# Optimization experiments

Measured on AMD Instinct MI355X. Metric: run time of the kernel, lower is better.

Reference implementation:

```python
import math
import jax, jax.numpy as jnp
import numpy as np

N, S, E, H = 8, 1024, 768, 12  # batch, seq_len, n_embed, n_head


def setup_inputs() -> dict:
    key = jax.random.key(0)
    ks = jax.random.split(key, 10)
    s = 1.0 / math.sqrt(E)
    x = jax.random.normal(ks[0], (N, S, E), dtype=jnp.float32)
    # per-head full-width projections, stacked over heads: [H, E, E] (Linear weight layout [out, in])
    Wq = jax.random.normal(ks[1], (H, E, E), dtype=jnp.float32) * s
    Wk = jax.random.normal(ks[2], (H, E, E), dtype=jnp.float32) * s
    Wv = jax.random.normal(ks[3], (H, E, E), dtype=jnp.float32) * s
    bq = jax.random.normal(ks[4], (H, E), dtype=jnp.float32) * s
    bk = jax.random.normal(ks[5], (H, E), dtype=jnp.float32) * s
    bv = jax.random.normal(ks[6], (H, E), dtype=jnp.float32) * s
    Wc = jax.random.normal(ks[7], (E, H * E), dtype=jnp.float32) * (1.0 / math.sqrt(H * E))
    bc = jax.random.normal(ks[8], (E,), dtype=jnp.float32) * s
    return {"x": x, "Wq": Wq, "bq": bq, "Wk": Wk, "bk": bk, "Wv": Wv, "bv": bv, "Wc": Wc, "bc": bc}


def reference(x, Wq, bq, Wk, bk, Wv, bv, Wc, bc):
    # Full-width QKV per head: [H, N, S, E]
    q = jnp.einsum('nse,hde->hnsd', x, Wq) + bq[:, None, None, :]
    k = jnp.einsum('nse,hde->hnsd', x, Wk) + bk[:, None, None, :]
    v = jnp.einsum('nse,hde->hnsd', x, Wv) + bv[:, None, None, :]
    # scores scaled by sqrt(n_embed) (source quirk: full n_embed, not head_dim)
    scores = jnp.einsum('hnsd,hntd->hnst', q, k) / math.sqrt(E)
    causal = jnp.tril(jnp.ones((S, S), dtype=bool))
    scores = jnp.where(causal[None, None, :, :], scores, -jnp.inf)
    # dropout applied before softmax in source; p=0 (eval) -> identity
    attn = jax.nn.softmax(scores, axis=-1)
    heads = jnp.einsum('hnst,hntd->hnsd', attn, v)  # [H, N, S, E]
    concat = jnp.transpose(heads, (1, 2, 0, 3)).reshape(N, S, H * E)
    return concat @ Wc.T + bc
```

## Files before the change

### kernel.cpp

```cpp
#include <hip/hip_runtime.h>
#include <hip/hip_bf16.h>
#include <stdint.h>

#define SEQ    1024
#define NBAT   8
#define EMB    768
#define NHEAD  12
#define MROWS  (NBAT*SEQ)
#define SCALE_S 0.03608439182435161f

typedef unsigned short u16;
typedef __attribute__((ext_vector_type(8))) short bf16x8;
typedef __attribute__((ext_vector_type(4))) float f32x4;

typedef void __attribute__((address_space(1)))* gas_ptr;
typedef void __attribute__((address_space(3)))* las_ptr;

__device__ __forceinline__ void gload16(const void* g, void* l) {
  __builtin_amdgcn_global_load_lds((gas_ptr)(void*)g, (las_ptr)l, 16, 0, 0);
}

#define VMCNT0 asm volatile("s_waitcnt vmcnt(0)" ::: "memory")
#define VMCNT2 asm volatile("s_waitcnt vmcnt(2)" ::: "memory")
#define VMCNT4 asm volatile("s_waitcnt vmcnt(4)" ::: "memory")
#define LGKM0  asm volatile("s_waitcnt lgkmcnt(0)" ::: "memory")
#define BARRIER asm volatile("s_barrier" ::: "memory")

__device__ __forceinline__ u16 f2bf(float f) {
  union { float f; uint32_t u; } a; a.f = f;
  uint32_t r = a.u + 0x7fffu + ((a.u >> 16) & 1u);
  return (u16)(r >> 16);
}
__device__ __forceinline__ uint32_t pack2(float a, float b) {
  return (uint32_t)f2bf(a) | ((uint32_t)f2bf(b) << 16);
}

__global__ void k_cvt(const float* __restrict__ s, u16* __restrict__ d, long n) {
  long i = ((long)blockIdx.x*blockDim.x + threadIdx.x)*8;
  if (i >= n) return;
  float4 a = *(const float4*)(s+i);
  float4 b = *(const float4*)(s+i+4);
  uint4 o; o.x = pack2(a.x,a.y); o.y = pack2(a.z,a.w);
  o.z = pack2(b.x,b.y); o.w = pack2(b.z,b.w);
  *(uint4*)(d+i) = o;
}

__global__ void k_cvt3(const float* __restrict__ s0, const float* __restrict__ s1,
                       const float* __restrict__ s2, u16* __restrict__ d0,
                       u16* __restrict__ d1, u16* __restrict__ d2, long n) {
  const float* s = blockIdx.z == 0 ? s0 : (blockIdx.z == 1 ? s1 : s2);
  u16* d = blockIdx.z == 0 ? d0 : (blockIdx.z == 1 ? d1 : d2);
  long i = ((long)blockIdx.x*blockDim.x + threadIdx.x)*8;
  if (i >= n) return;
  float4 a = *(const float4*)(s+i);
  float4 b = *(const float4*)(s+i+4);
  uint4 o; o.x = pack2(a.x,a.y); o.y = pack2(a.z,a.w);
  o.z = pack2(b.x,b.y); o.w = pack2(b.z,b.w);
  *(uint4*)(d+i) = o;
}

__global__ void k_cvtwc(const float* __restrict__ wc, u16* __restrict__ d, int Gi, int h0) {
  long ncol = (long)Gi*EMB;
  long i = ((long)blockIdx.x*blockDim.x + threadIdx.x)*4;
  if (i >= 768*ncol) return;
  long eo = i / ncol, c = i - eo*ncol;
  long g = c / EMB, dd = c - g*EMB;
  const float* s = wc + eo*(long)(NHEAD*EMB) + (h0+g)*EMB + dd;
  float4 a = *(const float4*)s;
  uint2 o; o.x = pack2(a.x,a.y); o.y = pack2(a.z,a.w);
  *(uint2*)(d+i) = o;
}

__global__ __launch_bounds__(512, 2) void k_gemm256(
    const u16* __restrict__ A, int lda,
    const u16* __restrict__ B, int ldb, int K,
    u16* __restrict__ Cb, long c_hs, int ldc,
    const float* __restrict__ bias, const float* __restrict__ bias2,
    int gsplit, int mode)
{
  __shared__ u16 lsA[2*16384];
  __shared__ u16 lsB[2*16384];

  int m0 = blockIdx.x * 256;
  int n0 = blockIdx.y * 256;
  int tid = threadIdx.x;
  int w = tid >> 6, l = tid & 63;
  int wr = w >> 2, wc = w & 3;

  const u16* gA = A + (size_t)(m0 + 32*w + (l>>3))*lda + (((l&7) ^ (l>>3)) << 3);
  const u16* gB = B + (size_t)(n0 + 32*w + (l>>3))*ldb + (((l&7) ^ (l>>3)) << 3);

#define STAGE256(t, buf) do { \
    int k0_ = (t)*64; \
    _Pragma("unroll") \
    for (int c_ = 0; c_ < 4; ++c_) \
      gload16(gA + (size_t)(c_*8)*lda + k0_, lsA + (buf)*16384 + (32*w + 8*c_)*64); \
    _Pragma("unroll") \
    for (int c_ = 0; c_ < 4; ++c_) \
      gload16(gB + (size_t)(c_*8)*ldb + k0_, lsB + (buf)*16384 + (32*w + 8*c_)*64); \
  } while(0)

  f32x4 acc[8][4];
  #pragma unroll
  for (int i = 0; i < 8; ++i)
    #pragma unroll
    for (int j = 0; j < 4; ++j) acc[i][j] = (f32x4)0.0f;

  int nt = K >> 6;
  STAGE256(0, 0);
  for (int t = 0; t < nt; ++t) {
    VMCNT0; BARRIER;
    if (t + 1 < nt) STAGE256(t+1, (t+1)&1);
    const u16* la = lsA + (t&1)*16384;
    const u16* lb = lsB + (t&1)*16384;
    #pragma unroll
    for (int ks = 0; ks < 2; ++ks) {
      int off = (((4*ks + (l>>4)) ^ (l&7)) << 3);
      bf16x8 af[8], bf_[4];
      #pragma unroll
      for (int fi = 0; fi < 8; ++fi)
        af[fi] = *(const bf16x8*)(la + (wr*128 + fi*16 + (l&15))*64 + off);
      #pragma unroll
      for (int fj = 0; fj < 4; ++fj)
        bf_[fj] = *(const bf16x8*)(lb + (wc*64 + fj*16 + (l&15))*64 + off);
      __builtin_amdgcn_s_setprio(1);
      #pragma unroll
      for (int fi = 0; fi < 8; ++fi)
        #pragma unroll
        for (int fj = 0; fj < 4; ++fj)
          acc[fi][fj] = __builtin_amdgcn_mfma_f32_16x16x32_bf16(af[fi], bf_[fj], acc[fi][fj], 0, 0, 0);
      __builtin_amdgcn_s_setprio(0);
    }
  }
#undef STAGE256

  if (mode == 0) {
    int s = n0 / 768;
    int dbase = n0 - s*768 + wc*64;
    const float* bsl = (s < gsplit) ? bias + (size_t)s*768 : bias2 + (size_t)(s - gsplit)*768;
    u16* Cs = Cb + (size_t)s*c_hs;
    #pragma unroll
    for (int fj = 0; fj < 4; ++fj) {
      int dcol = dbase + fj*16 + (l&15);
      float bb = bsl[dcol];
      #pragma unroll
      for (int fi = 0; fi < 8; ++fi) {
        #pragma unroll
        for (int r = 0; r < 4; ++r) {
          int row = m0 + wr*128 + fi*16 + (l>>4)*4 + r;
          Cs[(size_t)row*768 + dcol] = f2bf(acc[fi][fj][r] + bb);
        }
      }
    }
  } else {
    #pragma unroll
    for (int fi = 0; fi < 8; ++fi) {
      #pragma unroll
      for (int r = 0; r < 4; ++r) {
        int row = m0 + wr*128 + fi*16 + (l>>4)*4 + r;
        float bb = bias[row];
        #pragma unroll
        for (int fj = 0; fj < 4; ++fj) {
          int cbn = n0 + wc*64 + fj*16 + (l&15);
          Cb[(size_t)row*ldc + cbn] = f2bf(acc[fi][fj][r] + bb);
        }
      }
    }
  }
}

__global__ __launch_bounds__(256) void k_gemm(
    const u16* __restrict__ A, long a_hs, int lda,
    const u16* __restrict__ B, long b_hs, int ldb, int K,
    u16* Cb, float* Cf, long c_hs, int ldc,
    const float* __restrict__ bias, const float* __restrict__ bias2,
    long bias_hs, int gsplit, int mode, int swapxy)
{
  __shared__ u16 lsA[3*4096];
  __shared__ u16 lsB[3*4096];
  int g = blockIdx.z;
  const u16* Ag = A + (long)g*a_hs;
  const u16* Bg = B + (long)g*b_hs;
  int tm = swapxy ? blockIdx.y : blockIdx.x;
  int tn = swapxy ? blockIdx.x : blockIdx.y;
  int m0 = tm*128, n0 = tn*128;
  int tid = threadIdx.x;
  int w = tid >> 6, l = tid & 63;

  int srow = l >> 2;
  int scol = ((l & 3) ^ ((l >> 3) & 3)) * 8;
  const u16* ga0 = Ag + (long)(m0 + (2*w)*16   + srow)*lda + scol;
  const u16* ga1 = Ag + (long)(m0 + (2*w+1)*16 + srow)*lda + scol;
  const u16* gb0 = Bg + (long)(n0 + (2*w)*16   + srow)*ldb + scol;
  const u16* gb1 = Bg + (long)(n0 + (2*w+1)*16 + srow)*ldb + scol;

#define GSTAGE(k0, buf) do { \
    gload16(ga0 + (k0), lsA + (buf)*4096 + (2*w)*512); \
    gload16(ga1 + (k0), lsA + (buf)*4096 + (2*w+1)*512); \
    gload16(gb0 + (k0), lsB + (buf)*4096 + (2*w)*512); \
    gload16(gb1 + (k0), lsB + (buf)*4096 + (2*w+1)*512); \
  } while(0)

  f32x4 acc[4][4];
  #pragma unroll
  for (int i = 0; i < 4; ++i)
    #pragma unroll
    for (int j = 0; j < 4; ++j) acc[i][j] = (f32x4)0.0f;

  int wr = w >> 1, wc_ = w & 1;
  int frow = l & 15;
  int sp = (l >> 4) ^ ((frow >> 1) & 3);
  int aoff[4], boff[4];
  #pragma unroll
  for (int i = 0; i < 4; ++i) {
    aoff[i] = (wr*64 + i*16 + frow)*32 + sp*8;
    boff[i] = (wc_*64 + i*16 + frow)*32 + sp*8;
  }

  int nt = K >> 5;
  GSTAGE(0, 0);
  GSTAGE(32, 1);
  VMCNT4; BARRIER;
  int cur = 0;
  for (int t = 0; t < nt; ++t) {
    if (t + 2 < nt) {
      int nb = cur + 2; if (nb >= 3) nb -= 3;
      GSTAGE((t+2) << 5, nb);
    }
    const u16* la = lsA + cur*4096;
    const u16* lb = lsB + cur*4096;
    bf16x8 af[4], bfr[4];
    #pragma unroll
    for (int i = 0; i < 4; ++i) af[i] = *(const bf16x8*)(la + aoff[i]);
    #pragma unroll
    for (int j = 0; j < 4; ++j) bfr[j] = *(const bf16x8*)(lb + boff[j]);
    #pragma unroll
    for (int i = 0; i < 4; ++i)
      #pragma unroll
      for (int j = 0; j < 4; ++j)
        acc[i][j] = __builtin_amdgcn_mfma_f32_16x16x32_bf16(af[i], bfr[j], acc[i][j], 0, 0, 0);
    if (t + 2 < nt) { VMCNT4; } else { VMCNT0; }
    LGKM0; BARRIER;
    cur = (cur == 2) ? 0 : cur + 1;
  }
#undef GSTAGE

  u16* Cbg = Cb ? Cb + (long)g*c_hs : (u16*)0;
  const float* bsel = (g < gsplit) ? bias : bias2;
  long gi = (g < gsplit) ? g : g - gsplit;
  const float* bs = bsel ? bsel + gi*bias_hs : (const float*)0;
  int rl = (l >> 4)*4, cl = l & 15;
  #pragma unroll
  for (int i = 0; i < 4; ++i) {
    #pragma unroll
    for (int j = 0; j < 4; ++j) {
      int rb = m0 + wr*64 + i*16 + rl;
      int cb = n0 + wc_*64 + j*16 + cl;
      float cbv = 0.f;
      if ((mode == 0 || mode == 2) && bs) cbv = bs[cb];
      #pragma unroll
      for (int r = 0; r < 4; ++r) {
        int rr = rb + r;
        float v = acc[i][j][r];
        v += (mode == 1) ? bs[rr] : cbv;
        size_t idx = (size_t)rr*(size_t)ldc + cb;
        if (mode <= 1) Cbg[idx] = f2bf(v);
        else if (mode == 2) Cf[idx] = v;
        else Cf[idx] += v;
      }
    }
  }
}

__global__ __launch_bounds__(512, 2) void k_attn(
    const u16* __restrict__ qb, const u16* __restrict__ kb,
    const u16* __restrict__ vtb, u16* __restrict__ hb, int ldh)
{
  __shared__ u16 kls[3*8192];
  __shared__ u16 vls[3*8192];
  __shared__ float s_t[64*68];
  __shared__ u16 p_t[64*64];
  __shared__ float e_s[64];

  int b = blockIdx.x;
  int xcd = b & 7, kk_ = b >> 3;
  int gn = xcd + 8*(kk_ >> 3), pair = kk_ & 7;
  int g = gn >> 3, n = gn & 7;

  const u16* Q  = qb  + (size_t)g*MROWS*EMB + (size_t)n*SEQ*EMB;
  const u16* Kp = kb  + (size_t)g*MROWS*EMB + (size_t)n*SEQ*EMB;
  const u16* Vt = vtb + (size_t)g*EMB*MROWS + (size_t)n*SEQ;
  u16* H = hb + (size_t)(n*SEQ)*ldh + (size_t)g*EMB;

  int tid = threadIdx.x;
  int w = tid >> 6, l = tid & 63;
  int qg = w >> 1;
  int cg = w & 1;
  int frow = l & 15;
  int fsw = frow & 7;
  int srow = tid >> 3;
  int sphys = tid & 7;
  int scol = ((sphys ^ (srow & 7)) << 3);

#define KSTAGE(base, pc, buf) do { \
    gload16((base) + (pc)*128,      kls + (buf)*8192 + w*512); \
    gload16((base) + (pc)*128 + 64, kls + (buf)*8192 + 4096 + w*512); \
  } while(0)
#define VSTAGE(vc, buf) do { \
    gload16(Vs + (size_t)((vc)*128)*MROWS,      vls + (buf)*8192 + w*512); \
    gload16(Vs + (size_t)((vc)*128 + 64)*MROWS, vls + (buf)*8192 + 4096 + w*512); \
  } while(0)

  for (int half = 0; half < 2; ++half) {
    int qt = half ? 15 - pair : pair;
    int q0 = qt * 64;
    int nt = qt + 1;

    f32x4 acc[6][4];
    #pragma unroll
    for (int i = 0; i < 6; ++i)
      #pragma unroll
      for (int j = 0; j < 4; ++j) acc[i][j] = (f32x4)0.0f;
    float m_reg = -1e30f, l_reg = 0.f;

    const u16* Qs = Q + (size_t)(q0 + srow)*EMB + scol;
    bf16x8 qreg[12][2];
    KSTAGE(Qs, 0, 0);
    KSTAGE(Qs, 1, 1);
    VMCNT2; BARRIER;
    #pragma unroll
    for (int pc = 0; pc < 6; ++pc) {
      if (pc < 4) KSTAGE(Qs, pc+2, (pc+2)%3);
      const u16* qb_ = kls + (pc%3)*8192;
      #pragma unroll
      for (int kk2 = 0; kk2 < 2; ++kk2)
        #pragma unroll
        for (int kkl = 0; kkl < 2; ++kkl)
          qreg[2*pc + kk2][kkl] = *(const bf16x8*)(qb_ + kk2*4096 + (qg*16 + frow)*64
                                                   + (((kkl*4 + (l>>4)) ^ fsw) << 3));
      if (pc < 4) { VMCNT2; } else if (pc == 4) { VMCNT0; }
      LGKM0; BARRIER;
    }

    for (int tt = 0; tt < nt; ++tt) {
      int t0 = tt*64;
      const u16* Ks = Kp + (size_t)(t0 + srow)*EMB + scol;
      const u16* Vs = Vt + (size_t)srow*MROWS + t0 + scol;
      if (tt == 0) { KSTAGE(Ks, 0, 0); KSTAGE(Ks, 1, 1); }
      VMCNT2; BARRIER;

      f32x4 sacc[2]; sacc[0] = (f32x4)0.0f; sacc[1] = (f32x4)0.0f;
      #pragma unroll
      for (int c = 0; c < 6; ++c) {
        if (c < 4)       KSTAGE(Ks, c+2, (c+2)%3);
        else if (c == 4) VSTAGE(0, 0);
        else             VSTAGE(1, 1);
        const u16* kb_ = kls + (c%3)*8192;
        __builtin_amdgcn_s_setprio(1);
        #pragma unroll
        for (int kk2 = 0; kk2 < 2; ++kk2) {
          #pragma unroll
          for (int kkl = 0; kkl < 2; ++kkl) {
            int so = ((kkl*4 + (l>>4)) ^ fsw) << 3;
            bf16x8 aq = qreg[2*c + kk2][kkl];
            #pragma unroll
            for (int cc = 0; cc < 2; ++cc) {
              bf16x8 bk_ = *(const bf16x8*)(kb_ + kk2*4096 + ((cg*2 + cc)*16 + frow)*64 + so);
              sacc[cc] = __builtin_amdgcn_mfma_f32_16x16x32_bf16(aq, bk_, sacc[cc], 0, 0, 0);
            }
          }
        }
        __builtin_amdgcn_s_setprio(0);
        if (c < 5) { VMCNT2; LGKM0; BARRIER; }
      }

      #pragma unroll
      for (int cc = 0; cc < 2; ++cc)
        #pragma unroll
        for (int r = 0; r < 4; ++r)
          s_t[(qg*16 + (l>>4)*4 + r)*68 + cg*32 + cc*16 + (l&15)] = sacc[cc][r]*SCALE_S;
      LGKM0; BARRIER;
      {
        int qglob = q0 + srow;
        int cbase = t0 + sphys*8;
        float v[8]; float mx = -1e30f;
        #pragma unroll
        for (int j = 0; j < 8; ++j) {
          float s = s_t[srow*68 + sphys*8 + j];
          if (cbase + j > qglob) s = -1e30f;
          v[j] = s; mx = fmaxf(mx, s);
        }
        mx = fmaxf(mx, __shfl_xor(mx, 1));
        mx = fmaxf(mx, __shfl_xor(mx, 2));
        mx = fmaxf(mx, __shfl_xor(mx, 4));
        float mn = fmaxf(m_reg, mx);
        float esc = __expf(m_reg - mn);
        float ps = 0.f; u16 pk[8];
        #pragma unroll
        for (int j = 0; j < 8; ++j) { float p = __expf(v[j] - mn); ps += p; pk[j] = f2bf(p); }
        ps += __shfl_xor(ps, 1); ps += __shfl_xor(ps, 2); ps += __shfl_xor(ps, 4);
        l_reg = l_reg*esc + ps; m_reg = mn;
        if (sphys == 0) e_s[srow] = esc;
        uint4 pv;
        pv.x = (uint32_t)pk[0] | ((uint32_t)pk[1] << 16);
        pv.y = (uint32_t)pk[2] | ((uint32_t)pk[3] << 16);
        pv.z = (uint32_t)pk[4] | ((uint32_t)pk[5] << 16);
        pv.w = (uint32_t)pk[6] | ((uint32_t)pk[7] << 16);
        *(uint4*)(p_t + srow*64 + ((sphys ^ (srow & 7)) << 3)) = pv;
      }
      VMCNT2; LGKM0; BARRIER;
      float er[4];
      #pragma unroll
      for (int r = 0; r < 4; ++r) er[r] = e_s[qg*16 + (l>>4)*4 + r];
      #pragma unroll
      for (int i = 0; i < 6; ++i)
        #pragma unroll
        for (int j = 0; j < 4; ++j)
          #pragma unroll
          for (int r = 0; r < 4; ++r) acc[i][j][r] *= er[r];
      bf16x8 pa[2];
      #pragma unroll
      for (int kk = 0; kk < 2; ++kk)
        pa[kk] = *(const bf16x8*)(p_t + (qg*16 + frow)*64 + (((kk*4 + (l>>4)) ^ fsw) << 3));
      bool stage_next = (tt + 1 < nt);
      const u16* Ks2 = Kp + (size_t)(t0 + 64 + srow)*EMB + scol;
      #pragma unroll
      for (int c = 0; c < 6; ++c) {
        if (c < 4)            VSTAGE(c+2, (c+2)%3);
        else if (stage_next)  { if (c == 4) KSTAGE(Ks2, 0, 0); else KSTAGE(Ks2, 1, 1); }
        const u16* vb_ = vls + (c%3)*8192;
        __builtin_amdgcn_s_setprio(1);
        #pragma unroll
        for (int cf = 0; cf < 4; ++cf) {
          #pragma unroll
          for (int kk = 0; kk < 2; ++kk) {
            bf16x8 vbf = *(const bf16x8*)(vb_ + (cg*64 + cf*16 + frow)*64 + (((kk*4 + (l>>4)) ^ fsw) << 3));
            acc[c][cf] = __builtin_amdgcn_mfma_f32_16x16x32_bf16(pa[kk], vbf, acc[c][cf], 0, 0, 0);
          }
        }
        __builtin_amdgcn_s_setprio(0);
        if (c < 4)      { VMCNT2; LGKM0; BARRIER; }
        else if (c == 4){ if (stage_next) { VMCNT2; } else { VMCNT0; } LGKM0; BARRIER; }
      }
    }
    if (sphys == 0) e_s[srow] = l_reg;
    LGKM0; BARRIER;
    float linv[4];
    #pragma unroll
    for (int r = 0; r < 4; ++r) linv[r] = 1.0f / e_s[qg*16 + (l>>4)*4 + r];
    #pragma unroll
    for (int i = 0; i < 6; ++i)
      #pragma unroll
      for (int j = 0; j < 4; ++j) {
        int col = i*128 + cg*64 + j*16 + (l & 15);
        #pragma unroll
        for (int r = 0; r < 4; ++r) {
          int row = q0 + qg*16 + (l>>4)*4 + r;
          H[(size_t)row*ldh + col] = f2bf(acc[i][j][r]*linv[r]);
        }
      }
    BARRIER;
  }
#undef KSTAGE
#undef VSTAGE
}

extern "C" void kernel_launch(void* const* d_in, const int* in_sizes, int n_in,
                              void* d_out, int out_size, void* d_ws, size_t ws_size,
                              hipStream_t stream) {
  const float* x  = (const float*)d_in[0];
  const float* Wq = (const float*)d_in[1];
  const float* bq = (const float*)d_in[2];
  const float* Wk = (const float*)d_in[3];
  const float* bk = (const float*)d_in[4];
  const float* Wv = (const float*)d_in[5];
  const float* bv = (const float*)d_in[6];
  const float* Wc = (const float*)d_in[7];
  const float* bc = (const float*)d_in[8];
  float* out = (float*)d_out;

  const size_t XB  = (size_t)MROWS*EMB*sizeof(u16);
  const size_t WHB = (size_t)EMB*EMB*sizeof(u16);
  const size_t per_g = 4*WHB + 4*XB;
  long long avail = (long long)ws_size - (long long)XB - 4096;
  int G = (int)(avail / (long long)per_g);
  if (G < 1) G = 1;
  if (G > NHEAD) G = NHEAD;

  char* ws = (char*)d_ws;
  u16* xb  = (u16*)ws;  ws += XB;
  u16* wqb = (u16*)ws;  ws += (size_t)(2*G)*WHB;
  u16* wvb = (u16*)ws;  ws += (size_t)G*WHB;
  u16* wcb = (u16*)ws;  ws += (size_t)G*WHB;
  u16* qb  = (u16*)ws;  ws += (size_t)(2*G)*XB;
  u16* vtb = (u16*)ws;  ws += (size_t)G*XB;
  u16* hbf = (u16*)ws;  ws += (size_t)G*XB;

  k_cvt<<<dim3(3072), dim3(256), 0, stream>>>(x, xb, (long)MROWS*EMB);

  for (int h0 = 0; h0 < NHEAD; h0 += G) {
    int Gi = (G < NHEAD - h0) ? G : (NHEAD - h0);
    long nw = (long)Gi*EMB*EMB;
    k_cvt3<<<dim3((unsigned)(nw/8/256), 1, 3), dim3(256), 0, stream>>>(
        Wq + (size_t)h0*EMB*EMB, Wk + (size_t)h0*EMB*EMB, Wv + (size_t)h0*EMB*EMB,
        wqb, wqb + (size_t)Gi*EMB*EMB, wvb, nw);
    k_cvtwc<<<dim3((unsigned)((768L*Gi*EMB/4)/256)), dim3(256), 0, stream>>>(Wc, wcb, Gi, h0);
    k_gemm256<<<dim3(32, 6*Gi), dim3(512), 0, stream>>>(
        xb, EMB, wqb, EMB, EMB,
        qb, (long)MROWS*EMB, 768,
        bq + (size_t)h0*EMB, bk + (size_t)h0*EMB, Gi, 0);
    k_gemm256<<<dim3(3*Gi, 32), dim3(512), 0, stream>>>(
        wvb, EMB, xb, EMB, EMB,
        vtb, 0L, MROWS,
        bv + (size_t)h0*EMB, (const float*)0, 9999, 1);
    k_attn<<<dim3(8*NBAT*Gi), dim3(512), 0, stream>>>(
        qb, qb + (size_t)Gi*MROWS*EMB, vtb, hbf, Gi*EMB);
    k_gemm<<<dim3(64, 6, 1), dim3(256), 0, stream>>>(
        hbf, 0L, Gi*EMB, wcb, 0L, Gi*EMB, Gi*EMB,
        (u16*)0, out, 0L, EMB,
        (h0 == 0 ? bc : (const float*)0), (const float*)0, 0L, 9999,
        (h0 == 0 ? 2 : 3), 0);
  }
}
```

Measured before the change: 1.144 ms.

## Fold Wq^T·Wk into per-head matrix, skip K projection, drop key bias

Rewrites the scores algebraically as (x M + bq Wk) x^T with M = Wq^T Wk computed per head. The separate K projection GEMM goes away, keys come straight from the bf16 x, and the bq-dependent term becomes a per-key scalar added to the scores. Terms constant along each softmax row (bk and its cross terms) are dropped because softmax cancels them. This costs extra small kernels: a transposing weight conversion, a 768x768 M GEMM per head, and two GEMV kernels. Rounding M to bf16 may also change numerics.

```diff
diff --git a/kernel.cpp b/kernel.cpp
--- a/kernel.cpp
+++ b/kernel.cpp
@@ -30,6 +30,9 @@
   union { float f; uint32_t u; } a; a.f = f;
   uint32_t r = a.u + 0x7fffu + ((a.u >> 16) & 1u);
   return (u16)(r >> 16);
+}
+__device__ __forceinline__ float bf2f(u16 b) {
+  union { uint32_t u; float f; } c; c.u = (uint32_t)b << 16; return c.f;
 }
 __device__ __forceinline__ uint32_t pack2(float a, float b) {
   return (uint32_t)f2bf(a) | ((uint32_t)f2bf(b) << 16);
@@ -45,18 +48,27 @@
   *(uint4*)(d+i) = o;
 }
 
-__global__ void k_cvt3(const float* __restrict__ s0, const float* __restrict__ s1,
-                       const float* __restrict__ s2, u16* __restrict__ d0,
-                       u16* __restrict__ d1, u16* __restrict__ d2, long n) {
-  const float* s = blockIdx.z == 0 ? s0 : (blockIdx.z == 1 ? s1 : s2);
-  u16* d = blockIdx.z == 0 ? d0 : (blockIdx.z == 1 ? d1 : d2);
-  long i = ((long)blockIdx.x*blockDim.x + threadIdx.x)*8;
-  if (i >= n) return;
-  float4 a = *(const float4*)(s+i);
-  float4 b = *(const float4*)(s+i+4);
-  uint4 o; o.x = pack2(a.x,a.y); o.y = pack2(a.z,a.w);
-  o.z = pack2(b.x,b.y); o.w = pack2(b.z,b.w);
-  *(uint4*)(d+i) = o;
+__global__ void k_cvtT(const float* __restrict__ wq, const float* __restrict__ wk,
+                       u16* __restrict__ dq, u16* __restrict__ dk, int Gi) {
+  __shared__ float t[64][65];
+  int z = blockIdx.z;
+  const float* src = (z < Gi) ? wq + (size_t)z*EMB*EMB : wk + (size_t)(z-Gi)*EMB*EMB;
+  u16* dst = (z < Gi) ? dq + (size_t)z*EMB*EMB : dk + (size_t)(z-Gi)*EMB*EMB;
+  int d0 = blockIdx.x*64, e0 = blockIdx.y*64;
+  int tt = threadIdx.x;
+  int el = tt & 63, db = tt >> 6;
+  #pragma unroll
+  for (int p = 0; p < 16; ++p) {
+    int dl = p*4 + db;
+    t[dl][el] = src[(size_t)(d0+dl)*EMB + e0 + el];
+  }
+  __syncthreads();
+  int dl2 = tt & 63, eb = tt >> 6;
+  #pragma unroll
+  for (int p = 0; p < 16; ++p) {
+    int e2 = p*4 + eb;
+    dst[(size_t)(e0+e2)*EMB + d0 + dl2] = f2bf(t[dl2][e2]);
+  }
 }
 
 __global__ void k_cvtwc(const float* __restrict__ wc, u16* __restrict__ d, int Gi, int h0) {
@@ -71,6 +83,35 @@
   *(uint2*)(d+i) = o;
 }
 
+__global__ void k_mka(const u16* __restrict__ wkT, const float* __restrict__ bq,
+                      float* __restrict__ a) {
+  int g = blockIdx.y;
+  int e = blockIdx.x*256 + threadIdx.x;
+  const u16* row = wkT + (size_t)g*EMB*EMB + (size_t)e*EMB;
+  const float* b = bq + (size_t)g*EMB;
+  float s = 0.f;
+  for (int d = 0; d < EMB; ++d) s += bf2f(row[d]) * b[d];
+  a[(size_t)g*EMB + e] = s;
+}
+
+__global__ void k_mkv(const u16* __restrict__ xb, const float* __restrict__ a,
+                      float* __restrict__ v) {
+  int g = blockIdx.y;
+  int w = threadIdx.x >> 6, l = threadIdx.x & 63;
+  int i = blockIdx.x*8 + w;
+  const u16* xr = xb + (size_t)i*EMB;
+  const float* ag = a + (size_t)g*EMB;
+  float s = 0.f;
+  #pragma unroll
+  for (int c = 0; c < 12; ++c) {
+    int e = c*64 + l;
+    s += bf2f(xr[e]) * ag[e];
+  }
+  s += __shfl_xor(s, 1); s += __shfl_xor(s, 2); s += __shfl_xor(s, 4);
+  s += __shfl_xor(s, 8); s += __shfl_xor(s, 16); s += __shfl_xor(s, 32);
+  if (l == 0) v[(size_t)g*MROWS + i] = s;
+}
+
 __global__ __launch_bounds__(512, 2) void k_gemm256(
     const u16* __restrict__ A, int lda,
     const u16* __restrict__ B, int ldb, int K,
@@ -137,12 +178,14 @@
   if (mode == 0) {
     int s = n0 / 768;
     int dbase = n0 - s*768 + wc*64;
-    const float* bsl = (s < gsplit) ? bias + (size_t)s*768 : bias2 + (size_t)(s - gsplit)*768;
+    const float* bsl = bias ? ((s < gsplit) ? bias + (size_t)s*768
+                                            : bias2 + (size_t)(s - gsplit)*768)
+                            : (const float*)0;
     u16* Cs = Cb + (size_t)s*c_hs;
     #pragma unroll
     for (int fj = 0; fj < 4; ++fj) {
       int dcol = dbase + fj*16 + (l&15);
-      float bb = bsl[dcol];
+      float bb = bsl ? bsl[dcol] : 0.f;
       #pragma unroll
       for (int fi = 0; fi < 8; ++fi) {
         #pragma unroll
@@ -273,8 +316,9 @@
 }
 
 __global__ __launch_bounds__(512, 2) void k_attn(
-    const u16* __restrict__ qb, const u16* __restrict__ kb,
-    const u16* __restrict__ vtb, u16* __restrict__ hb, int ldh)
+    const u16* __restrict__ qb, const u16* __restrict__ xkb,
+    const u16* __restrict__ vtb, const float* __restrict__ vh,
+    u16* __restrict__ hb, int ldh)
 {
   __shared__ u16 kls[3*8192];
   __shared__ u16 vls[3*8192];
@@ -288,8 +332,9 @@
   int g = gn >> 3, n = gn & 7;
 
   const u16* Q  = qb  + (size_t)g*MROWS*EMB + (size_t)n*SEQ*EMB;
-  const u16* Kp = kb  + (size_t)g*MROWS*EMB + (size_t)n*SEQ*EMB;
+  const u16* Kp = xkb + (size_t)n*SEQ*EMB;
   const u16* Vt = vtb + (size_t)g*EMB*MROWS + (size_t)n*SEQ;
+  const float* Vh = vh + (size_t)g*MROWS + (size_t)n*SEQ;
   u16* H = hb + (size_t)(n*SEQ)*ldh + (size_t)g*EMB;
 
   int tid = threadIdx.x;
@@ -346,6 +391,8 @@
       int t0 = tt*64;
       const u16* Ks = Kp + (size_t)(t0 + srow)*EMB + scol;
       const u16* Vs = Vt + (size_t)srow*MROWS + t0 + scol;
+      float vv0 = Vh[t0 + cg*32 + frow];
+      float vv1 = Vh[t0 + cg*32 + 16 + frow];
       if (tt == 0) { KSTAGE(Ks, 0, 0); KSTAGE(Ks, 1, 1); }
       VMCNT2; BARRIER;
 
@@ -375,10 +422,10 @@
       }
 
       #pragma unroll
-      for (int cc = 0; cc < 2; ++cc)
-        #pragma unroll
-        for (int r = 0; r < 4; ++r)
-          s_t[(qg*16 + (l>>4)*4 + r)*68 + cg*32 + cc*16 + (l&15)] = sacc[cc][r]*SCALE_S;
+      for (int r = 0; r < 4; ++r) {
+        s_t[(qg*16 + (l>>4)*4 + r)*68 + cg*32 + frow]      = (sacc[0][r] + vv0)*SCALE_S;
+        s_t[(qg*16 + (l>>4)*4 + r)*68 + cg*32 + 16 + frow] = (sacc[1][r] + vv1)*SCALE_S;
+      }
       LGKM0; BARRIER;
       {
         int qglob = q0 + srow;
@@ -472,49 +519,62 @@
   const float* Wq = (const float*)d_in[1];
   const float* bq = (const float*)d_in[2];
   const float* Wk = (const float*)d_in[3];
-  const float* bk = (const float*)d_in[4];
+  const float* bv = (const float*)d_in[6];
   const float* Wv = (const float*)d_in[5];
-  const float* bv = (const float*)d_in[6];
   const float* Wc = (const float*)d_in[7];
   const float* bc = (const float*)d_in[8];
   float* out = (float*)d_out;
 
   const size_t XB  = (size_t)MROWS*EMB*sizeof(u16);
   const size_t WHB = (size_t)EMB*EMB*sizeof(u16);
-  const size_t per_g = 4*WHB + 4*XB;
-  long long avail = (long long)ws_size - (long long)XB - 4096;
-  int G = (int)(avail / (long long)per_g);
-  if (G < 1) G = 1;
-  if (G > NHEAD) G = NHEAD;
+  const size_t VHB = (size_t)MROWS*sizeof(float);
+  const size_t AB  = (size_t)EMB*sizeof(float);
+  const size_t per_g = 3*WHB + 3*XB + VHB + AB;
+  int G = 4;
+  { int cands[4] = {4, 3, 2, 1};
+    for (int ci = 0; ci < 4; ++ci) {
+      G = cands[ci];
+      if (XB + (size_t)G*per_g + 4096 <= ws_size) break;
+    } }
 
   char* ws = (char*)d_ws;
   u16* xb  = (u16*)ws;  ws += XB;
-  u16* wqb = (u16*)ws;  ws += (size_t)(2*G)*WHB;
   u16* wvb = (u16*)ws;  ws += (size_t)G*WHB;
   u16* wcb = (u16*)ws;  ws += (size_t)G*WHB;
-  u16* qb  = (u16*)ws;  ws += (size_t)(2*G)*XB;
+  u16* mtb = (u16*)ws;  ws += (size_t)G*WHB;
+  u16* yb  = (u16*)ws;  ws += (size_t)G*XB;
   u16* vtb = (u16*)ws;  ws += (size_t)G*XB;
   u16* hbf = (u16*)ws;  ws += (size_t)G*XB;
+  float* vh = (float*)ws; ws += (size_t)G*VHB;
+  float* ab = (float*)ws; ws += (size_t)G*AB;
+  u16* wqT = hbf;
+  u16* wkT = hbf + (size_t)G*EMB*EMB;
 
   k_cvt<<<dim3(3072), dim3(256), 0, stream>>>(x, xb, (long)MROWS*EMB);
 
   for (int h0 = 0; h0 < NHEAD; h0 += G) {
     int Gi = (G < NHEAD - h0) ? G : (NHEAD - h0);
-    long nw = (long)Gi*EMB*EMB;
-    k_cvt3<<<dim3((unsigned)(nw/8/256), 1, 3), dim3(256), 0, stream>>>(
-        Wq + (size_t)h0*EMB*EMB, Wk + (size_t)h0*EMB*EMB, Wv + (size_t)h0*EMB*EMB,
-        wqb, wqb + (size_t)Gi*EMB*EMB, wvb, nw);
+    k_cvtT<<<dim3(12, 12, 2*Gi), dim3(256), 0, stream>>>(
+        Wq + (size_t)h0*EMB*EMB, Wk + (size_t)h0*EMB*EMB, wqT, wkT, Gi);
+    k_cvt<<<dim3((unsigned)((long)Gi*EMB*EMB/8/256)), dim3(256), 0, stream>>>(
+        Wv + (size_t)h0*EMB*EMB, wvb, (long)Gi*EMB*EMB);
     k_cvtwc<<<dim3((unsigned)((768L*Gi*EMB/4)/256)), dim3(256), 0, stream>>>(Wc, wcb, Gi, h0);
-    k_gemm256<<<dim3(32, 6*Gi), dim3(512), 0, stream>>>(
-        xb, EMB, wqb, EMB, EMB,
-        qb, (long)MROWS*EMB, 768,
-        bq + (size_t)h0*EMB, bk + (size_t)h0*EMB, Gi, 0);
+    k_gemm<<<dim3(6, 6, Gi), dim3(256), 0, stream>>>(
+        wkT, (long)EMB*EMB, EMB, wqT, (long)EMB*EMB, EMB, EMB,
+        mtb, (float*)0, (long)EMB*EMB, EMB,
+        (const float*)0, (const float*)0, 0L, 9999, 0, 0);
+    k_mka<<<dim3(3, Gi), dim3(256), 0, stream>>>(wkT, bq + (size_t)h0*EMB, ab);
+    k_mkv<<<dim3(1024, Gi), dim3(512), 0, stream>>>(xb, ab, vh);
+    k_gemm256<<<dim3(32, 3*Gi), dim3(512), 0, stream>>>(
+        xb, EMB, mtb, EMB, EMB,
+        yb, (long)MROWS*EMB, 768,
+        (const float*)0, (const float*)0, Gi, 0);
     k_gemm256<<<dim3(3*Gi, 32), dim3(512), 0, stream>>>(
         wvb, EMB, xb, EMB, EMB,
         vtb, 0L, MROWS,
         bv + (size_t)h0*EMB, (const float*)0, 9999, 1);
     k_attn<<<dim3(8*NBAT*Gi), dim3(512), 0, stream>>>(
-        qb, qb + (size_t)Gi*MROWS*EMB, vtb, hbf, Gi*EMB);
+        yb, xb, vtb, vh, hbf, Gi*EMB);
     k_gemm<<<dim3(64, 6, 1), dim3(256), 0, stream>>>(
         hbf, 0L, Gi*EMB, wcb, 0L, Gi*EMB, Gi*EMB,
         (u16*)0, out, 0L, EMB,
```

New measurement: 1.206 ms. 1.05x slower.
